# Performance work log

Hardware: AMD Instinct MI355X
Metric: run time of the kernel (lower is better)

The kernel has to match this reference:

```python
import jax, jax.numpy as jnp
import numpy as np

IN, HID, RANK, B = 2048, 2048, 512, 8192


def setup_inputs() -> dict:
    key = jax.random.key(0)
    ks = jax.random.split(key, 16)
    s_in = 1.0 / np.sqrt(IN + HID)
    s_r = 1.0 / np.sqrt(RANK)
    inp = {
        "x": jax.random.normal(ks[0], (B, IN), jnp.float32),
        "h": jax.random.normal(ks[1], (B, HID), jnp.float32),
        "c": jax.random.normal(ks[2], (B, HID), jnp.float32),
    }
    names = ["i", "f", "c", "o"]
    for idx, g in enumerate(names):
        inp[f"U{g}"] = jax.random.uniform(ks[3 + 3 * idx], (IN + HID, RANK), jnp.float32, -s_in, s_in)
        inp[f"V{g}"] = jax.random.uniform(ks[4 + 3 * idx], (RANK, HID), jnp.float32, -s_r, s_r)
        inp[f"b{g}"] = jnp.zeros((HID,), jnp.float32)
    return inp


def reference(x, h, c, Ui, Vi, bi, Uf, Vf, bf, Uc, Vc, bc, Uo, Vo, bo):
    combined = jnp.concatenate([x, h], axis=1)  # [B, IN+HID]

    def gate(U, V, b):
        return (combined @ U) @ V + b  # low-rank: [B,R] then [B,HID]

    i = jax.nn.sigmoid(gate(Ui, Vi, bi))
    f = jax.nn.sigmoid(gate(Uf, Vf, bf))
    o = jax.nn.sigmoid(gate(Uo, Vo, bo))
    c_hat = jnp.tanh(gate(Uc, Vc, bc))
    c_new = f * c + i * c_hat
    h_new = o * jnp.tanh(c_new)
    return (h_new, c_new)
```

## Files before the change

### kernel.cpp

```cpp
#include <hip/hip_runtime.h>
#include <hip/hip_bf16.h>
#include <cstdint>
#include <cstddef>

typedef __bf16 bf16;
typedef __bf16 bf16x8 __attribute__((ext_vector_type(8)));
typedef float f32x4 __attribute__((ext_vector_type(4)));

#define BATCH 8192
#define IN_DIM 2048
#define HID 2048
#define RANK 512
#define KDIM 4096
#define NG 2048
#define CHUNK_ROWS 4096


__device__ __forceinline__ void gload16(const void* g, void* l) {
  __builtin_amdgcn_global_load_lds(
      (const __attribute__((address_space(1))) unsigned int*)g,
      (__attribute__((address_space(3))) unsigned int*)l, 16, 0, 0);
}

__device__ __forceinline__ float sigmoidf_(float x) {
  return 1.0f / (1.0f + __expf(-x));
}
__device__ __forceinline__ float tanhf_(float x) {
  return 1.0f - 2.0f / (__expf(2.0f * x) + 1.0f);
}

__device__ __forceinline__ void stage_half(const bf16* __restrict__ g0, int ld,
                                           int row0, int kcol, bf16* lbase, int tid) {
  const int wid = tid >> 6;
  #pragma unroll
  for (int q = 0; q < 2; ++q) {
    const int slot = q * 512 + tid;
    const int row = slot >> 3, cb = slot & 7;
    const int gcb = cb ^ (row & 7);
    gload16(g0 + (size_t)(row0 + row) * ld + kcol + gcb * 8,
            lbase + (size_t)(q * 64 + wid * 8) * 64);
  }
}

#define GBAR  __builtin_amdgcn_s_barrier()
#define LGKM0 asm volatile("s_waitcnt lgkmcnt(0)" ::: "memory")
#define VMC4  asm volatile("s_waitcnt vmcnt(4)" ::: "memory")

#define LD_B(BUFc)                                                                   \
  _Pragma("unroll") for (int j = 0; j < 4; ++j) {                                    \
    b[j][0] = *(const bf16x8*)(&Bls[BUFc][wn + j * 16 + lr][(lk ^ sw) * 8]);         \
    b[j][1] = *(const bf16x8*)(&Bls[BUFc][wn + j * 16 + lr][((4 | lk) ^ sw) * 8]);   \
  }
#define LD_A(BUFc, Q)                                                                \
  _Pragma("unroll") for (int ai = 0; ai < 2; ++ai) {                                 \
    a[ai][0] = *(const bf16x8*)(&Als[BUFc][wm + ((Q) * 2 + ai) * 16 + lr][(lk ^ sw) * 8]); \
    a[ai][1] = *(const bf16x8*)(&Als[BUFc][wm + ((Q) * 2 + ai) * 16 + lr][((4 | lk) ^ sw) * 8]); \
  }
#define MFMAQ(Q)                                                                     \
  _Pragma("unroll") for (int ai = 0; ai < 2; ++ai)                                   \
  _Pragma("unroll") for (int ks = 0; ks < 2; ++ks)                                   \
  _Pragma("unroll") for (int j = 0; j < 4; ++j)                                      \
    acc[(Q) * 2 + ai][j] = __builtin_amdgcn_mfma_f32_16x16x32_bf16(                  \
        a[ai][ks], b[j][ks], acc[(Q) * 2 + ai][j], 0, 0, 0);

#define PHASE(BUFc, Q, STAGE, TAILVM) \
  {                                   \
    if ((Q) == 0) { LD_B(BUFc); }     \
    LD_A(BUFc, Q);                    \
    STAGE;                            \
    GBAR;                             \
    LGKM0;                            \
    __builtin_amdgcn_s_setprio(1);    \
    MFMAQ(Q);                         \
    __builtin_amdgcn_s_setprio(0);    \
    TAILVM;                           \
    GBAR;                             \
  }

template <int NT>
__device__ __forceinline__ void gemm_core(const bf16* __restrict__ A, int lda, int m0,
                                          const bf16* __restrict__ B, int ldb, int n0,
                                          bf16 (&Als)[2][256][64], bf16 (&Bls)[2][256][64],
                                          f32x4 (&acc)[8][4]) {
  const int tid = threadIdx.x;
  const int wid = tid >> 6, lane = tid & 63;
  const int wm = (wid >> 2) * 128, wn = (wid & 3) * 64;
  const int lr = lane & 15, lk = lane >> 4;
  const int sw = lr & 7;
  bf16x8 a[2][2], b[4][2];

  #pragma unroll
  for (int i = 0; i < 8; ++i)
    #pragma unroll
    for (int j = 0; j < 4; ++j) acc[i][j] = (f32x4){0.f, 0.f, 0.f, 0.f};

  stage_half(A, lda, m0,       0,  &Als[0][0][0],   tid);
  stage_half(A, lda, m0 + 128, 0,  &Als[0][128][0], tid);
  stage_half(B, ldb, n0,       0,  &Bls[0][0][0],   tid);
  stage_half(B, ldb, n0 + 128, 0,  &Bls[0][128][0], tid);
  stage_half(B, ldb, n0,       64, &Bls[1][0][0],   tid);
  stage_half(B, ldb, n0 + 128, 64, &Bls[1][128][0], tid);
  VMC4;
  GBAR;

  for (int t = 0; t < NT / 2; ++t) {
    const int c = 2 * t;
    const int kc1 = ((c + 1) & (NT - 1)) * 64;
    const int kc2 = ((c + 2) & (NT - 1)) * 64;
    const int kc3 = ((c + 3) & (NT - 1)) * 64;
    PHASE(0, 0, stage_half(A, lda, m0,       kc1, &Als[1][0][0],   tid), (void)0);
    PHASE(0, 1, stage_half(A, lda, m0 + 128, kc1, &Als[1][128][0], tid), (void)0);
    PHASE(0, 2, stage_half(B, ldb, n0,       kc2, &Bls[0][0][0],   tid), (void)0);
    PHASE(0, 3, stage_half(B, ldb, n0 + 128, kc2, &Bls[0][128][0], tid), VMC4);
    PHASE(1, 0, stage_half(A, lda, m0,       kc2, &Als[0][0][0],   tid), (void)0);
    PHASE(1, 1, stage_half(A, lda, m0 + 128, kc2, &Als[0][128][0], tid), (void)0);
    PHASE(1, 2, stage_half(B, ldb, n0,       kc3, &Bls[1][0][0],   tid), (void)0);
    PHASE(1, 3, stage_half(B, ldb, n0 + 128, kc3, &Bls[1][128][0], tid), VMC4);
  }
}


__global__ void k_convert_combined(const float* __restrict__ x,
                                   const float* __restrict__ h,
                                   bf16* __restrict__ out) {
  size_t i4 = (size_t)blockIdx.x * blockDim.x + threadIdx.x;
  size_t base = i4 * 4;
  int col = (int)(base & (KDIM - 1));
  size_t row = base >> 12;
  const float* src = (col < IN_DIM) ? (x + row * IN_DIM + col)
                                    : (h + row * (size_t)HID + (col - IN_DIM));
  float4 v = *(const float4*)src;
  union { bf16 b[4]; uint2 u; } p;
  p.b[0] = (bf16)v.x; p.b[1] = (bf16)v.y; p.b[2] = (bf16)v.z; p.b[3] = (bf16)v.w;
  *(uint2*)(out + base) = p.u;
}


__global__ void k_tconv4(const float* __restrict__ s0, const float* __restrict__ s1,
                         const float* __restrict__ s2, const float* __restrict__ s3,
                         bf16* __restrict__ out, int nrow, int ncol,
                         long ostride, long gstride) {
  __shared__ float t[32][33];
  const float* in = blockIdx.z == 0 ? s0 : blockIdx.z == 1 ? s1
                  : blockIdx.z == 2 ? s2 : s3;
  bf16* o = out + (size_t)blockIdx.z * gstride;
  int c0 = blockIdx.x * 32, r0 = blockIdx.y * 32;
  int tx = threadIdx.x, ty = threadIdx.y;
  #pragma unroll
  for (int yy = ty; yy < 32; yy += 8)
    t[yy][tx] = in[(size_t)(r0 + yy) * ncol + c0 + tx];
  __syncthreads();
  #pragma unroll
  for (int yy = ty; yy < 32; yy += 8)
    o[(size_t)(c0 + yy) * ostride + r0 + tx] = (bf16)t[tx][yy];
}


__launch_bounds__(512, 2)
__global__ void k_gemm1(const bf16* __restrict__ A,
                        const bf16* __restrict__ Bt,
                        bf16* __restrict__ R) {
  __shared__ __align__(16) bf16 Als[2][256][64];
  __shared__ __align__(16) bf16 Bls[2][256][64];
  const int bx = blockIdx.x;
  const int id = (bx & 7) * 32 + (bx >> 3);
  const int m0 = (id >> 3) * 256, n0 = (id & 7) * 256;
  f32x4 acc[8][4];
  gemm_core<KDIM / 64>(A, KDIM, m0, Bt, KDIM, n0, Als, Bls, acc);

  const int tid = threadIdx.x;
  const int wid = tid >> 6, lane = tid & 63;
  const int wm = (wid >> 2) * 128, wn = (wid & 3) * 64;
  const int lr = lane & 15, lk = lane >> 4;
  #pragma unroll
  for (int i = 0; i < 8; ++i)
    #pragma unroll
    for (int j = 0; j < 4; ++j)
      #pragma unroll
      for (int v = 0; v < 4; ++v)
        R[(size_t)(m0 + wm + i * 16 + lk * 4 + v) * NG + (n0 + wn + j * 16 + lr)] =
            (bf16)acc[i][j][v];
}


__launch_bounds__(512, 2)
__global__ void k_gates(const bf16* __restrict__ Rb,
                        const bf16* __restrict__ Vt,
                        const float* __restrict__ b0, const float* __restrict__ b1,
                        const float* __restrict__ b2, const float* __restrict__ b3,
                        bf16* __restrict__ G, int m_base) {
  __shared__ __align__(16) bf16 Als[2][256][64];
  __shared__ __align__(16) bf16 Bls[2][256][64];
  const int bx = blockIdx.x;
  const int id = (bx & 7) * 64 + (bx >> 3);
  const int gate = id >> 7;
  const int mo = ((id >> 3) & 15) * 256;
  const int n0 = (id & 7) * 256;
  f32x4 acc[8][4];
  gemm_core<RANK / 64>(Rb + gate * RANK, NG, m_base + mo,
                       Vt + (size_t)gate * HID * RANK, RANK, n0, Als, Bls, acc);

  const int tid = threadIdx.x;
  const int wid = tid >> 6, lane = tid & 63;
  const int wm = (wid >> 2) * 128, wn = (wid & 3) * 64;
  const int lr = lane & 15, lk = lane >> 4;
  const float* bias = gate == 0 ? b0 : gate == 1 ? b1 : gate == 2 ? b2 : b3;
  const bool is_tanh = (gate == 2);
  bf16* Gg = G + (size_t)gate * CHUNK_ROWS * HID;
  #pragma unroll
  for (int j = 0; j < 4; ++j) {
    const int col = n0 + wn + j * 16 + lr;
    const float bj = bias[col];
    #pragma unroll
    for (int i = 0; i < 8; ++i)
      #pragma unroll
      for (int v = 0; v < 4; ++v) {
        const int row = mo + wm + i * 16 + lk * 4 + v;
        float p = acc[i][j][v] + bj;
        float av = is_tanh ? tanhf_(p) : sigmoidf_(p);
        Gg[(size_t)row * HID + col] = (bf16)av;
      }
  }
}


__global__ void k_ew(const bf16* __restrict__ G,
                     const float* __restrict__ cin,
                     float* __restrict__ hout, float* __restrict__ cout,
                     int m_base) {
  const size_t CHUNK = (size_t)CHUNK_ROWS * HID;
  const bf16* Gi = G;
  const bf16* Gf = G + CHUNK;
  const bf16* Gc = G + 2 * CHUNK;
  const bf16* Go = G + 3 * CHUNK;
  const size_t n8 = CHUNK / 8;
  for (size_t t = (size_t)blockIdx.x * blockDim.x + threadIdx.x; t < n8;
       t += (size_t)gridDim.x * blockDim.x) {
    size_t e = t * 8;
    bf16x8 vi = *(const bf16x8*)(Gi + e);
    bf16x8 vf = *(const bf16x8*)(Gf + e);
    bf16x8 vc = *(const bf16x8*)(Gc + e);
    bf16x8 vo = *(const bf16x8*)(Go + e);
    size_t ge = (size_t)m_base * HID + e;
    float4 c0 = *(const float4*)(cin + ge);
    float4 c1 = *(const float4*)(cin + ge + 4);
    float cc[8] = {c0.x, c0.y, c0.z, c0.w, c1.x, c1.y, c1.z, c1.w};
    float cn[8], hn[8];
    #pragma unroll
    for (int v = 0; v < 8; ++v) {
      float iv = (float)vi[v], fv = (float)vf[v], cv = (float)vc[v], ov = (float)vo[v];
      cn[v] = fv * cc[v] + iv * cv;
      hn[v] = ov * tanhf_(cn[v]);
    }
    *(float4*)(cout + ge)     = (float4){cn[0], cn[1], cn[2], cn[3]};
    *(float4*)(cout + ge + 4) = (float4){cn[4], cn[5], cn[6], cn[7]};
    *(float4*)(hout + ge)     = (float4){hn[0], hn[1], hn[2], hn[3]};
    *(float4*)(hout + ge + 4) = (float4){hn[4], hn[5], hn[6], hn[7]};
  }
}


extern "C" void kernel_launch(void* const* d_in, const int* in_sizes, int n_in,
                              void* d_out, int out_size, void* d_ws, size_t ws_size,
                              hipStream_t stream) {
  const float* x = (const float*)d_in[0];
  const float* h = (const float*)d_in[1];
  const float* c = (const float*)d_in[2];
  const float* U[4] = {(const float*)d_in[3], (const float*)d_in[6],
                       (const float*)d_in[9], (const float*)d_in[12]};
  const float* V[4] = {(const float*)d_in[4], (const float*)d_in[7],
                       (const float*)d_in[10], (const float*)d_in[13]};
  const float* b[4] = {(const float*)d_in[5], (const float*)d_in[8],
                       (const float*)d_in[11], (const float*)d_in[14]};

  char* ws = (char*)d_ws;
  bf16* combined = (bf16*)ws;
  bf16* Ut       = (bf16*)(ws + 67108864);
  bf16* Vt       = (bf16*)(ws + 67108864 + 16777216);
  bf16* Rbuf     = (bf16*)(ws + 67108864 + 16777216 + 8388608);
  bf16* G        = (bf16*)ws;

  float* hout = (float*)d_out;
  float* cout = hout + (size_t)BATCH * HID;

  k_convert_combined<<<(BATCH * (size_t)KDIM / 4) / 256, 256, 0, stream>>>(x, h, combined);

  k_tconv4<<<dim3(RANK / 32, KDIM / 32, 4), dim3(32, 8), 0, stream>>>(
      U[0], U[1], U[2], U[3], Ut, KDIM, RANK, KDIM, (long)RANK * KDIM);
  k_tconv4<<<dim3(HID / 32, RANK / 32, 4), dim3(32, 8), 0, stream>>>(
      V[0], V[1], V[2], V[3], Vt, RANK, HID, RANK, (long)HID * RANK);

  k_gemm1<<<256, 512, 0, stream>>>(combined, Ut, Rbuf);

  for (int chunk = 0; chunk < 2; ++chunk) {
    int m_base = chunk * CHUNK_ROWS;
    k_gates<<<512, 512, 0, stream>>>(Rbuf, Vt, b[0], b[1], b[2], b[3], G, m_base);
    k_ew<<<2048, 256, 0, stream>>>(G, c, hout, cout, m_base);
  }
}
```

Baseline: 395.1 us.

## Triple-buffer B tiles and prefetch LDS fragments during MFMA phases

Restructures the GEMM mainloop to use a flat LDS buffer with two A stages and three rotating B stages, staging B two k-steps ahead. A and B fragment reads for the next phase are issued right after each MFMA block rather than before the barrier, with sched_barrier fences, to hide LDS read latency behind compute. This raises LDS use per block to 160 KB, which on a 160 KB LDS would drop occupancy from 2 blocks/CU to 1 despite the launch bounds.

```diff
diff --git a/kernel.cpp b/kernel.cpp
--- a/kernel.cpp
+++ b/kernel.cpp
@@ -45,43 +45,47 @@
 #define GBAR  __builtin_amdgcn_s_barrier()
 #define LGKM0 asm volatile("s_waitcnt lgkmcnt(0)" ::: "memory")
 #define VMC4  asm volatile("s_waitcnt vmcnt(4)" ::: "memory")
-
-#define LD_B(BUFc)                                                                   \
-  _Pragma("unroll") for (int j = 0; j < 4; ++j) {                                    \
-    b[j][0] = *(const bf16x8*)(&Bls[BUFc][wn + j * 16 + lr][(lk ^ sw) * 8]);         \
-    b[j][1] = *(const bf16x8*)(&Bls[BUFc][wn + j * 16 + lr][((4 | lk) ^ sw) * 8]);   \
-  }
-#define LD_A(BUFc, Q)                                                                \
-  _Pragma("unroll") for (int ai = 0; ai < 2; ++ai) {                                 \
-    a[ai][0] = *(const bf16x8*)(&Als[BUFc][wm + ((Q) * 2 + ai) * 16 + lr][(lk ^ sw) * 8]); \
-    a[ai][1] = *(const bf16x8*)(&Als[BUFc][wm + ((Q) * 2 + ai) * 16 + lr][((4 | lk) ^ sw) * 8]); \
-  }
-#define MFMAQ(Q)                                                                     \
-  _Pragma("unroll") for (int ai = 0; ai < 2; ++ai)                                   \
-  _Pragma("unroll") for (int ks = 0; ks < 2; ++ks)                                   \
-  _Pragma("unroll") for (int j = 0; j < 4; ++j)                                      \
-    acc[(Q) * 2 + ai][j] = __builtin_amdgcn_mfma_f32_16x16x32_bf16(                  \
+#define VMC8  asm volatile("s_waitcnt vmcnt(8)" ::: "memory")
+#define SB0   __builtin_amdgcn_sched_barrier(0)
+
+#define LD_Ap(PA, Q)                                                          \
+  _Pragma("unroll") for (int ai = 0; ai < 2; ++ai)                            \
+  _Pragma("unroll") for (int ks = 0; ks < 2; ++ks)                            \
+    a[ai][ks] = *(const bf16x8*)((PA) + (wm + (Q) * 32 + ai * 16 + lr) * 64   \
+                                 + ((((ks << 2) | lk) ^ sw) << 3));
+
+#define LD_Bp(PB)                                                             \
+  _Pragma("unroll") for (int j = 0; j < 4; ++j)                               \
+  _Pragma("unroll") for (int ks = 0; ks < 2; ++ks)                            \
+    b[j][ks] = *(const bf16x8*)((PB) + (wn + j * 16 + lr) * 64                \
+                                 + ((((ks << 2) | lk) ^ sw) << 3));
+
+#define MFMAQ(Q)                                                              \
+  _Pragma("unroll") for (int ai = 0; ai < 2; ++ai)                            \
+  _Pragma("unroll") for (int ks = 0; ks < 2; ++ks)                            \
+  _Pragma("unroll") for (int j = 0; j < 4; ++j)                               \
+    acc[(Q) * 2 + ai][j] = __builtin_amdgcn_mfma_f32_16x16x32_bf16(           \
         a[ai][ks], b[j][ks], acc[(Q) * 2 + ai][j], 0, 0, 0);
 
-#define PHASE(BUFc, Q, STAGE, TAILVM) \
-  {                                   \
-    if ((Q) == 0) { LD_B(BUFc); }     \
-    LD_A(BUFc, Q);                    \
-    STAGE;                            \
-    GBAR;                             \
-    LGKM0;                            \
-    __builtin_amdgcn_s_setprio(1);    \
-    MFMAQ(Q);                         \
-    __builtin_amdgcn_s_setprio(0);    \
-    TAILVM;                           \
-    GBAR;                             \
+#define PHASE3(TOP, STAGE, Q, PFOP, TAILVM) \
+  {                                         \
+    TOP;                                    \
+    STAGE;                                  \
+    GBAR;                                   \
+    LGKM0;                                  \
+    __builtin_amdgcn_s_setprio(1);          \
+    MFMAQ(Q);                               \
+    __builtin_amdgcn_s_setprio(0);          \
+    PFOP;                                   \
+    SB0;                                    \
+    TAILVM;                                 \
+    GBAR;                                   \
   }
 
 template <int NT>
 __device__ __forceinline__ void gemm_core(const bf16* __restrict__ A, int lda, int m0,
                                           const bf16* __restrict__ B, int ldb, int n0,
-                                          bf16 (&Als)[2][256][64], bf16 (&Bls)[2][256][64],
-                                          f32x4 (&acc)[8][4]) {
+                                          bf16* lds, f32x4 (&acc)[8][4]) {
   const int tid = threadIdx.x;
   const int wid = tid >> 6, lane = tid & 63;
   const int wm = (wid >> 2) * 128, wn = (wid & 3) * 64;
@@ -89,33 +93,44 @@
   const int sw = lr & 7;
   bf16x8 a[2][2], b[4][2];
 
+  bf16* Ab0 = lds;
+  bf16* Ab1 = lds + 16384;
+  bf16* Rg0 = lds + 2 * 16384;
+  bf16* Rg1 = lds + 3 * 16384;
+  bf16* Rg2 = lds + 4 * 16384;
+
   #pragma unroll
   for (int i = 0; i < 8; ++i)
     #pragma unroll
     for (int j = 0; j < 4; ++j) acc[i][j] = (f32x4){0.f, 0.f, 0.f, 0.f};
 
-  stage_half(A, lda, m0,       0,  &Als[0][0][0],   tid);
-  stage_half(A, lda, m0 + 128, 0,  &Als[0][128][0], tid);
-  stage_half(B, ldb, n0,       0,  &Bls[0][0][0],   tid);
-  stage_half(B, ldb, n0 + 128, 0,  &Bls[0][128][0], tid);
-  stage_half(B, ldb, n0,       64, &Bls[1][0][0],   tid);
-  stage_half(B, ldb, n0 + 128, 64, &Bls[1][128][0], tid);
-  VMC4;
+  stage_half(A, lda, m0,       0,   Ab0,        tid);
+  stage_half(A, lda, m0 + 128, 0,   Ab0 + 8192, tid);
+  stage_half(B, ldb, n0,       0,   Rg0,        tid);
+  stage_half(B, ldb, n0 + 128, 0,   Rg0 + 8192, tid);
+  stage_half(B, ldb, n0,       64,  Rg1,        tid);
+  stage_half(B, ldb, n0 + 128, 64,  Rg1 + 8192, tid);
+  stage_half(B, ldb, n0,       128, Rg2,        tid);
+  stage_half(B, ldb, n0 + 128, 128, Rg2 + 8192, tid);
+  VMC8;
   GBAR;
-
-  for (int t = 0; t < NT / 2; ++t) {
-    const int c = 2 * t;
+  LD_Bp(Rg0);
+
+  bf16 *pBc = Rg0, *pBn = Rg1, *pBn2 = Rg2;
+  bf16 *pAc = Ab0, *pAa = Ab1;
+  for (int c = 0; c < NT; ++c) {
     const int kc1 = ((c + 1) & (NT - 1)) * 64;
-    const int kc2 = ((c + 2) & (NT - 1)) * 64;
     const int kc3 = ((c + 3) & (NT - 1)) * 64;
-    PHASE(0, 0, stage_half(A, lda, m0,       kc1, &Als[1][0][0],   tid), (void)0);
-    PHASE(0, 1, stage_half(A, lda, m0 + 128, kc1, &Als[1][128][0], tid), (void)0);
-    PHASE(0, 2, stage_half(B, ldb, n0,       kc2, &Bls[0][0][0],   tid), (void)0);
-    PHASE(0, 3, stage_half(B, ldb, n0 + 128, kc2, &Bls[0][128][0], tid), VMC4);
-    PHASE(1, 0, stage_half(A, lda, m0,       kc2, &Als[0][0][0],   tid), (void)0);
-    PHASE(1, 1, stage_half(A, lda, m0 + 128, kc2, &Als[0][128][0], tid), (void)0);
-    PHASE(1, 2, stage_half(B, ldb, n0,       kc3, &Bls[1][0][0],   tid), (void)0);
-    PHASE(1, 3, stage_half(B, ldb, n0 + 128, kc3, &Bls[1][128][0], tid), VMC4);
+    PHASE3(LD_Ap(pAc, 0), stage_half(A, lda, m0,       kc1, pAa,        tid), 0,
+           LD_Ap(pAc, 1), (void)0);
+    PHASE3((void)0,       stage_half(A, lda, m0 + 128, kc1, pAa + 8192, tid), 1,
+           LD_Ap(pAc, 2), (void)0);
+    PHASE3((void)0,       stage_half(B, ldb, n0,       kc3, pBc,        tid), 2,
+           LD_Ap(pAc, 3), (void)0);
+    PHASE3((void)0,       stage_half(B, ldb, n0 + 128, kc3, pBc + 8192, tid), 3,
+           LD_Bp(pBn),    VMC4);
+    bf16* tt = pBc; pBc = pBn; pBn = pBn2; pBn2 = tt;
+    tt = pAc; pAc = pAa; pAa = tt;
   }
 }
 
@@ -160,13 +175,12 @@
 __global__ void k_gemm1(const bf16* __restrict__ A,
                         const bf16* __restrict__ Bt,
                         bf16* __restrict__ R) {
-  __shared__ __align__(16) bf16 Als[2][256][64];
-  __shared__ __align__(16) bf16 Bls[2][256][64];
+  __shared__ __align__(16) bf16 lds[81920];
   const int bx = blockIdx.x;
   const int id = (bx & 7) * 32 + (bx >> 3);
   const int m0 = (id >> 3) * 256, n0 = (id & 7) * 256;
   f32x4 acc[8][4];
-  gemm_core<KDIM / 64>(A, KDIM, m0, Bt, KDIM, n0, Als, Bls, acc);
+  gemm_core<KDIM / 64>(A, KDIM, m0, Bt, KDIM, n0, lds, acc);
 
   const int tid = threadIdx.x;
   const int wid = tid >> 6, lane = tid & 63;
@@ -189,8 +203,7 @@
                         const float* __restrict__ b0, const float* __restrict__ b1,
                         const float* __restrict__ b2, const float* __restrict__ b3,
                         bf16* __restrict__ G, int m_base) {
-  __shared__ __align__(16) bf16 Als[2][256][64];
-  __shared__ __align__(16) bf16 Bls[2][256][64];
+  __shared__ __align__(16) bf16 lds[81920];
   const int bx = blockIdx.x;
   const int id = (bx & 7) * 64 + (bx >> 3);
   const int gate = id >> 7;
@@ -198,7 +211,7 @@
   const int n0 = (id & 7) * 256;
   f32x4 acc[8][4];
   gemm_core<RANK / 64>(Rb + gate * RANK, NG, m_base + mo,
-                       Vt + (size_t)gate * HID * RANK, RANK, n0, Als, Bls, acc);
+                       Vt + (size_t)gate * HID * RANK, RANK, n0, lds, acc);
 
   const int tid = threadIdx.x;
   const int wid = tid >> 6, lane = tid & 63;
```

New measurement: 346.7 us. 12.2% less time.
